# Kernel optimization log

Measured on AMD Instinct MI355X. Metric: run time of the kernel, lower is better.

Reference implementation:

```python
import jax, jax.numpy as jnp
from jax import lax
import numpy as np

B, C_IN, C_OUT, H, W, K = 4, 128, 256, 64, 64, 3
KK = K * K
MID = C_IN // 4
EPS = 1e-5


def conv2d(x, w, b, pad, groups=1):
    out = lax.conv_general_dilated(x, w, (1, 1), [(pad, pad), (pad, pad)],
                                   feature_group_count=groups,
                                   dimension_numbers=('NCHW', 'OIHW', 'NCHW'))
    return out + b[None, :, None, None]


def bnorm(x, g, b, m, v):
    # inference-mode BatchNorm2d
    scale = (g / jnp.sqrt(v + EPS))
    return (x - m[None, :, None, None]) * scale[None, :, None, None] + b[None, :, None, None]


def bilinear_gather(x, py, px):
    # x: (B,C,H,W); py/px: (B,KK,H,W) float sample coords; zero outside bounds
    Bb, C, Hh, Ww = x.shape
    xf = x.reshape(Bb, C, Hh * Ww)
    y0 = jnp.floor(py)
    x0 = jnp.floor(px)
    wy1 = py - y0
    wx1 = px - x0

    def corner(yc, xc, wgt):
        valid = (yc >= 0) & (yc <= Hh - 1) & (xc >= 0) & (xc <= Ww - 1)
        yi = jnp.clip(yc, 0, Hh - 1).astype(jnp.int32)
        xi = jnp.clip(xc, 0, Ww - 1).astype(jnp.int32)
        idx = (yi * Ww + xi).reshape(Bb, -1)  # (B, KK*H*W)
        g = jax.vmap(lambda f, i: f[:, i])(xf, idx).reshape(Bb, C, *py.shape[1:])
        return g * (wgt * valid)[:, None]

    return (corner(y0, x0, (1 - wy1) * (1 - wx1))
            + corner(y0, x0 + 1, (1 - wy1) * wx1)
            + corner(y0 + 1, x0, wy1 * (1 - wx1))
            + corner(y0 + 1, x0 + 1, wy1 * wx1))


def deform_conv2d(x, offset, mask, w, b, pad=1):
    # modulated deformable conv v2, stride=1, dilation=1, groups=1, dg=1
    Bb, C, Hh, Ww = x.shape
    off = offset.reshape(Bb, KK, 2, Hh, Ww)  # (dy,dx) per kernel point
    k = jnp.arange(KK)
    ky = (k // K).astype(x.dtype)
    kx = (k % K).astype(x.dtype)
    py = (jnp.arange(Hh, dtype=x.dtype) - pad)[None, None, :, None] + ky[None, :, None, None] + off[:, :, 0]
    px = (jnp.arange(Ww, dtype=x.dtype) - pad)[None, None, None, :] + kx[None, :, None, None] + off[:, :, 1]
    val = bilinear_gather(x, py, px) * mask[:, None]  # (B,C,KK,H,W)
    return jnp.einsum('bckhw,ock->bohw', val, w.reshape(w.shape[0], C, KK)) + b[None, :, None, None]


def setup_inputs() -> dict:
    key = jax.random.key(0)
    ks = iter(jax.random.split(key, 40))

    def P(shape, scale=0.05):
        return jax.random.normal(next(ks), shape, jnp.float32) * scale

    d = {}
    d['x'] = jax.random.normal(next(ks), (B, C_IN, H, W), jnp.float32)
    # DCConv offset branch
    d['oc1_w'] = P((MID, C_IN, 3, 3)); d['oc1_b'] = P((MID,))
    d['obn_g'] = jnp.ones((MID,)); d['obn_b'] = jnp.zeros((MID,))
    d['obn_m'] = jnp.zeros((MID,)); d['obn_v'] = jnp.ones((MID,))
    d['oc2_w'] = P((2 * KK, MID, 3, 3), 0.01); d['oc2_b'] = P((2 * KK,), 0.01)
    # DCConv mask branch
    d['mc1_w'] = P((MID, C_IN, 3, 3)); d['mc1_b'] = P((MID,))
    d['mbn_g'] = jnp.ones((MID,)); d['mbn_b'] = jnp.zeros((MID,))
    d['mbn_m'] = jnp.zeros((MID,)); d['mbn_v'] = jnp.ones((MID,))
    d['mc2_w'] = P((KK, MID, 3, 3), 0.01); d['mc2_b'] = jnp.ones((KK,))
    # DCConv main weight
    d['dc_w'] = P((C_OUT, C_IN, 3, 3)); d['dc_b'] = jnp.zeros((C_OUT,))
    # contour branch: depthwise 3x3 + BN + ReLU + 1x1
    d['cb_dw_w'] = P((C_IN, 1, 3, 3)); d['cb_dw_b'] = P((C_IN,))
    d['cbn_g'] = jnp.ones((C_IN,)); d['cbn_b'] = jnp.zeros((C_IN,))
    d['cbn_m'] = jnp.zeros((C_IN,)); d['cbn_v'] = jnp.ones((C_IN,))
    d['cb_pw_w'] = P((C_OUT // 2, C_IN, 1, 1)); d['cb_pw_b'] = P((C_OUT // 2,))
    # spatial attention 7x7 -> 1 channel
    d['sa_w'] = P((1, C_OUT + C_OUT // 2, 7, 7)); d['sa_b'] = jnp.zeros((1,))
    # fusion 1x1 + BN + ReLU
    d['fu_w'] = P((C_OUT, C_OUT + C_OUT // 2, 1, 1)); d['fu_b'] = jnp.zeros((C_OUT,))
    d['fbn_g'] = jnp.ones((C_OUT,)); d['fbn_b'] = jnp.zeros((C_OUT,))
    d['fbn_m'] = jnp.zeros((C_OUT,)); d['fbn_v'] = jnp.ones((C_OUT,))
    return d


def reference(x, oc1_w, oc1_b, obn_g, obn_b, obn_m, obn_v, oc2_w, oc2_b,
              mc1_w, mc1_b, mbn_g, mbn_b, mbn_m, mbn_v, mc2_w, mc2_b,
              dc_w, dc_b, cb_dw_w, cb_dw_b, cbn_g, cbn_b, cbn_m, cbn_v,
              cb_pw_w, cb_pw_b, sa_w, sa_b, fu_w, fu_b, fbn_g, fbn_b, fbn_m, fbn_v):
    # DCConv: offsets + sigmoid masks + modulated deformable conv
    h = jax.nn.relu(bnorm(conv2d(x, oc1_w, oc1_b, 1), obn_g, obn_b, obn_m, obn_v))
    offset = conv2d(h, oc2_w, oc2_b, 1)
    hm = jax.nn.relu(bnorm(conv2d(x, mc1_w, mc1_b, 1), mbn_g, mbn_b, mbn_m, mbn_v))
    mask = jax.nn.sigmoid(conv2d(hm, mc2_w, mc2_b, 1))
    main_feat = deform_conv2d(x, offset, mask, dc_w, dc_b, pad=1)
    # contour branch
    hc = jax.nn.relu(bnorm(conv2d(x, cb_dw_w, cb_dw_b, 1, groups=C_IN), cbn_g, cbn_b, cbn_m, cbn_v))
    contour_feat = conv2d(hc, cb_pw_w, cb_pw_b, 0)
    combined = jnp.concatenate([main_feat, contour_feat], axis=1)
    attn = jax.nn.sigmoid(conv2d(combined, sa_w, sa_b, 3))
    combined = combined * attn
    return jax.nn.relu(bnorm(conv2d(combined, fu_w, fu_b, 0), fbn_g, fbn_b, fbn_m, fbn_v))
```

## Files before the change

### kernel.cpp

```cpp
#include <hip/hip_runtime.h>
#include <hip/hip_bf16.h>
#include <math.h>

#define BN   4
#define CIN  128
#define COUT 256
#define HWP  4096

typedef __hip_bfloat16 bf16;
typedef __attribute__((ext_vector_type(8))) short sh8;
typedef __attribute__((ext_vector_type(4))) float f32x4;

__device__ __forceinline__ float b2f(bf16 v) { return __bfloat162float(v); }
__device__ __forceinline__ float bflo(unsigned u) { return __uint_as_float(u << 16); }
__device__ __forceinline__ float bfhi(unsigned u) { return __uint_as_float(u & 0xffff0000u); }
__device__ __forceinline__ unsigned short f2bfbits(float f) {
    union { bf16 h; unsigned short u; } cv; cv.h = __float2bfloat16(f); return cv.u;
}
__device__ __forceinline__ float bfj(const uint4& c, int j) {
    unsigned u = (&c.x)[j >> 1];
    return (j & 1) ? bfhi(u) : bflo(u);
}

__global__ __launch_bounds__(256) void prep_all_kernel(
    const float* __restrict__ x, bf16* __restrict__ xt,
    const float* __restrict__ dc_w,
    const float* __restrict__ oc1_w, const float* __restrict__ oc1_b,
    const float* __restrict__ obn_g, const float* __restrict__ obn_b,
    const float* __restrict__ obn_m, const float* __restrict__ obn_v,
    const float* __restrict__ mc1_w, const float* __restrict__ mc1_b,
    const float* __restrict__ mbn_g, const float* __restrict__ mbn_b,
    const float* __restrict__ mbn_m, const float* __restrict__ mbn_v,
    const float* __restrict__ fu_w, const float* __restrict__ fu_b,
    const float* __restrict__ fbn_g, const float* __restrict__ fbn_b,
    const float* __restrict__ fbn_m, const float* __restrict__ fbn_v,
    const float* __restrict__ sa_w,
    const float* __restrict__ oc2_w, const float* __restrict__ mc2_w,
    const float* __restrict__ cb_pw_w,
    const float* __restrict__ cb_dw_b, const float* __restrict__ cbn_g,
    const float* __restrict__ cbn_b, const float* __restrict__ cbn_m,
    const float* __restrict__ cbn_v,
    bf16* __restrict__ wBf2, bf16* __restrict__ wCf2, float* __restrict__ ab,
    bf16* __restrict__ wFf, bf16* __restrict__ wSAf, float* __restrict__ fab,
    bf16* __restrict__ wDf, bf16* __restrict__ wPf, float* __restrict__ dwab)
{
    __shared__ bf16 t[64][136];
    if (blockIdx.x < 256) {
        const int b = blockIdx.x >> 6, chunk = blockIdx.x & 63;
        const int pos0 = chunk * 64;
        const int tid = threadIdx.x;
        const int lane = tid & 63, wv = tid >> 6;
        const float* xb = x + (size_t)b * CIN * HWP + pos0 + lane;
        #pragma unroll 4
        for (int j = 0; j < 32; j++) {
            int ci = wv * 32 + j;
            t[lane][ci] = __float2bfloat16(xb[(size_t)ci * HWP]);
        }
        __syncthreads();
        const int p = tid >> 2, cig = tid & 3;
        uint4* dst = (uint4*)(xt + ((size_t)b * HWP + pos0 + p) * 128 + cig * 32);
        const uint4* src = (const uint4*)&t[p][cig * 32];
        #pragma unroll
        for (int q = 0; q < 4; q++) dst[q] = src[q];
        return;
    }

    int o = (blockIdx.x - 256) * 256 + threadIdx.x;
    if (o < 294912) {
        int j = o & 7, o2 = o >> 3;
        int lane = o2 & 63, t_ = o2 >> 6;
        int l16 = lane & 15, quad = lane >> 4;
        int mt = t_ & 3, t2 = t_ >> 2;
        int kt = t2 % 18, t3 = t2 / 18;
        int h = t3 & 1, wv = t3 >> 1;
        int co = wv * 64 + mt * 16 + l16;
        int kkh = kt * 32 + quad * 8 + j;
        int k = kkh >> 6, ci = h * 64 + (kkh & 63);
        wBf2[o] = __float2bfloat16(dc_w[co * 1152 + ci * 9 + k]);
    } else if (o < 368640) {
        int idx = o - 294912;
        int j = idx & 7, o2 = idx >> 3;
        int lane = o2 & 63, t_ = o2 >> 6;
        int l16 = lane & 15, quad = lane >> 4;
        int kt = t_ % 18, t2 = t_ / 18;
        int h = t2 & 1, wv = t2 >> 1;
        int co = wv * 16 + l16;
        int kkh = kt * 32 + quad * 8 + j;
        int k = kkh >> 6, ci = h * 64 + (kkh & 63);
        float v = (co < 32) ? oc1_w[co * 1152 + ci * 9 + k]
                            : mc1_w[(co - 32) * 1152 + ci * 9 + k];
        wCf2[idx] = __float2bfloat16(v);
    } else if (o < 368704) {
        int c = o - 368640;
        float g, bb, m, vv, bias;
        if (c < 32) { g = obn_g[c]; bb = obn_b[c]; m = obn_m[c]; vv = obn_v[c]; bias = oc1_b[c]; }
        else { int c2 = c - 32; g = mbn_g[c2]; bb = mbn_b[c2]; m = mbn_m[c2]; vv = mbn_v[c2]; bias = mc1_b[c2]; }
        float alpha = g / sqrtf(vv + 1e-5f);
        ab[c] = alpha;
        ab[64 + c] = (bias - m) * alpha + bb;
    } else if (o < 467008) {
        int idx = o - 368704;
        int j = idx & 7, o2 = idx >> 3;
        int lane = o2 & 63, t_ = o2 >> 6;
        int l16 = lane & 15, quad = lane >> 4;
        int mt = t_ & 3, t2 = t_ >> 2;
        int kt = t2 % 12, wv = t2 / 12;
        int co = wv * 64 + mt * 16 + l16;
        int kk = kt * 32 + quad * 8 + j;
        wFf[idx] = __float2bfloat16(fu_w[co * 384 + kk]);
    } else if (o < 491584) {
        int idx = o - 467008;
        int j = idx & 7, o2 = idx >> 3;
        int lane = o2 & 63, t_ = o2 >> 6;
        int l16 = lane & 15, quad = lane >> 4;
        int kt = t_ % 12, wv = t_ / 12;
        int jr = wv * 16 + l16;
        int kk = kt * 32 + quad * 8 + j;
        wSAf[idx] = (jr < 49) ? __float2bfloat16(sa_w[kk * 49 + jr]) : __float2bfloat16(0.f);
    } else if (o < 491840) {
        int co = o - 491584;
        float alpha = fbn_g[co] / sqrtf(fbn_v[co] + 1e-5f);
        fab[co] = alpha;
        fab[256 + co] = (fu_b[co] - fbn_m[co]) * alpha + fbn_b[co];
    } else if (o < 510272) {
        int idx = o - 491840;
        int j = idx & 7, o2 = idx >> 3;
        int lane = o2 & 63, t_ = o2 >> 6;
        int l16 = lane & 15, quad = lane >> 4;
        int mt = t_ & 1, kt = t_ >> 1;
        int co = mt * 16 + l16;
        int kk = kt * 32 + quad * 8 + j;
        int k = kk >> 6, c = kk & 63;
        float v = 0.f;
        if (co < 18 && c < 32) v = oc2_w[co * 288 + c * 9 + k];
        else if (co >= 18 && co < 27 && c >= 32) v = mc2_w[(co - 18) * 288 + (c - 32) * 9 + k];
        wDf[idx] = __float2bfloat16(v);
    } else if (o < 526656) {
        int idx = o - 510272;
        int j = idx & 7, o2 = idx >> 3;
        int lane = o2 & 63, t_ = o2 >> 6;
        int l16 = lane & 15, quad = lane >> 4;
        int wv = t_ >> 3, kt = (t_ >> 1) & 3, mt = t_ & 1;
        int co = wv * 32 + mt * 16 + l16;
        int kk = kt * 32 + quad * 8 + j;
        wPf[idx] = __float2bfloat16(cb_pw_w[co * 128 + kk]);
    } else if (o < 526784) {
        int c = o - 526656;
        float alpha = cbn_g[c] / sqrtf(cbn_v[c] + 1e-5f);
        dwab[c] = alpha;
        dwab[128 + c] = (cb_dw_b[c] - cbn_m[c]) * alpha + cbn_b[c];
    }
}

__global__ __launch_bounds__(256) void conv1_mfma_kernel(
    const bf16* __restrict__ xt, const bf16* __restrict__ wCf2, const float* __restrict__ ab,
    bf16* __restrict__ ht)
{
    __shared__ __align__(16) bf16 val[32][584];

    const int bid = blockIdx.x;
    const int b = (bid & 7) >> 1;
    const int tile = ((bid >> 3) << 1) | (bid & 1);
    const int pos0 = tile * 32;
    const int y = tile >> 1, x0 = (tile & 1) * 32;
    const int tid = threadIdx.x;
    const int lane = tid & 63, wv = tid >> 6;
    const int quad = lane >> 4, l16 = lane & 15;

    f32x4 acc[2] = {f32x4{0,0,0,0}, f32x4{0,0,0,0}};
    const bf16* xtb = xt + (size_t)b * HWP * 128;

    #pragma unroll
    for (int h = 0; h < 2; h++) {
        if (h) __syncthreads();
        {
            const int cig = tid & 7, pix = tid >> 3;
            const int ci0 = h * 64 + cig * 8;
            const int xxp = x0 + pix;
            #pragma unroll
            for (int k = 0; k < 9; k++) {
                int yy = y + k / 3 - 1, xx = xxp + k % 3 - 1;
                bool valid = (yy >= 0 && yy <= 63 && xx >= 0 && xx <= 63);
                uint4 c = {0, 0, 0, 0};
                if (valid) c = *(const uint4*)(xtb + (size_t)(yy * 64 + xx) * 128 + ci0);
                *(uint4*)&val[pix][k * 64 + cig * 8] = c;
            }
        }
        __syncthreads();

        const bf16* wl0 = wCf2 + ((size_t)(wv * 2 + h) * 18) * 512 + lane * 8;
        const bf16* vb0 = &val[l16][quad * 8];
        const bf16* vb1 = &val[16 + l16][quad * 8];
        for (int kt = 0; kt < 18; kt++) {
            sh8 af = *(const sh8*)(wl0 + kt * 512);
            sh8 b0 = *(const sh8*)(vb0 + kt * 32);
            sh8 b1 = *(const sh8*)(vb1 + kt * 32);
            acc[0] = __builtin_amdgcn_mfma_f32_16x16x32_bf16(af, b0, acc[0], 0, 0, 0);
            acc[1] = __builtin_amdgcn_mfma_f32_16x16x32_bf16(af, b1, acc[1], 0, 0, 0);
        }
    }

    const int co0 = wv * 16 + quad * 4;
    #pragma unroll
    for (int ph = 0; ph < 2; ph++) {
        float o0 = fmaxf(acc[ph][0] * ab[co0 + 0] + ab[64 + co0 + 0], 0.f);
        float o1 = fmaxf(acc[ph][1] * ab[co0 + 1] + ab[64 + co0 + 1], 0.f);
        float o2 = fmaxf(acc[ph][2] * ab[co0 + 2] + ab[64 + co0 + 2], 0.f);
        float o3 = fmaxf(acc[ph][3] * ab[co0 + 3] + ab[64 + co0 + 3], 0.f);
        uint2 pk;
        pk.x = (unsigned)f2bfbits(o0) | ((unsigned)f2bfbits(o1) << 16);
        pk.y = (unsigned)f2bfbits(o2) | ((unsigned)f2bfbits(o3) << 16);
        *(uint2*)(ht + ((size_t)b * HWP + pos0 + ph * 16 + l16) * 64 + co0) = pk;
    }
}

__global__ __launch_bounds__(256) void dwpw_kernel(
    const bf16* __restrict__ xt, const float* __restrict__ dw_w, const float* __restrict__ dwab,
    const bf16* __restrict__ wPf, const float* __restrict__ pw_b,
    const bf16* __restrict__ wSAf, bf16* __restrict__ combined, float* __restrict__ part_b)
{
    __shared__ float wl[1152];
    __shared__ float abl[256];
    __shared__ __align__(16) bf16 vdw[16][136];
    const int bid = blockIdx.x;
    const int b = bid >> 8, tile = bid & 255;
    const int pos0 = tile * 16;
    const int y = tile >> 2, x0 = (tile & 3) * 16;
    const int tid = threadIdx.x;
    for (int i = tid; i < 1152; i += 256) wl[i] = dw_w[i];
    abl[tid] = dwab[tid];
    __syncthreads();

    {
        const int cig = tid & 15, pix = tid >> 4;
        const int ci0 = cig * 8;
        const int xxp = x0 + pix;
        const bf16* xtb = xt + (size_t)b * HWP * 128;
        float g[8] = {0, 0, 0, 0, 0, 0, 0, 0};
        #pragma unroll
        for (int k = 0; k < 9; k++) {
            int yy = y + k / 3 - 1, xx = xxp + k % 3 - 1;
            if (yy < 0 || yy > 63 || xx < 0 || xx > 63) continue;
            uint4 c = *(const uint4*)(xtb + (size_t)(yy * 64 + xx) * 128 + ci0);
            #pragma unroll
            for (int j = 0; j < 8; j++)
                g[j] += wl[(ci0 + j) * 9 + k] * bfj(c, j);
        }
        uint4 pk;
        float o[8];
        #pragma unroll
        for (int j = 0; j < 8; j++)
            o[j] = fmaxf(g[j] * abl[ci0 + j] + abl[128 + ci0 + j], 0.f);
        pk.x = (unsigned)f2bfbits(o[0]) | ((unsigned)f2bfbits(o[1]) << 16);
        pk.y = (unsigned)f2bfbits(o[2]) | ((unsigned)f2bfbits(o[3]) << 16);
        pk.z = (unsigned)f2bfbits(o[4]) | ((unsigned)f2bfbits(o[5]) << 16);
        pk.w = (unsigned)f2bfbits(o[6]) | ((unsigned)f2bfbits(o[7]) << 16);
        *(uint4*)&vdw[pix][ci0] = pk;
    }
    __syncthreads();

    const int lane = tid & 63, wv = tid >> 6;
    const int quad = lane >> 4, l16 = lane & 15;
    f32x4 acc[2] = {f32x4{0,0,0,0}, f32x4{0,0,0,0}};
    const bf16* fb = &vdw[l16][quad * 8];
    const bf16* wl0 = wPf + (size_t)wv * 4096 + lane * 8;
    #pragma unroll
    for (int kt = 0; kt < 4; kt++) {
        sh8 bf = *(const sh8*)(fb + kt * 32);
        #pragma unroll
        for (int mt = 0; mt < 2; mt++) {
            sh8 af = *(const sh8*)(wl0 + (kt * 2 + mt) * 512);
            acc[mt] = __builtin_amdgcn_mfma_f32_16x16x32_bf16(af, bf, acc[mt], 0, 0, 0);
        }
    }

    bf16* ct = combined + ((size_t)b * HWP + pos0 + l16) * 384 + 256;
    #pragma unroll
    for (int mt = 0; mt < 2; mt++) {
        int co_b = wv * 32 + mt * 16 + quad * 4;
        uint2 pk;
        pk.x = (unsigned)f2bfbits(acc[mt][0] + pw_b[co_b])     | ((unsigned)f2bfbits(acc[mt][1] + pw_b[co_b + 1]) << 16);
        pk.y = (unsigned)f2bfbits(acc[mt][2] + pw_b[co_b + 2]) | ((unsigned)f2bfbits(acc[mt][3] + pw_b[co_b + 3]) << 16);
        *(uint2*)(ct + co_b) = pk;
    }

    __syncthreads();
    bf16* ct2 = &vdw[0][0];
    #pragma unroll
    for (int mt = 0; mt < 2; mt++) {
        int co_b = wv * 32 + mt * 16 + quad * 4;
        uint2 pk;
        pk.x = (unsigned)f2bfbits(acc[mt][0] + pw_b[co_b])     | ((unsigned)f2bfbits(acc[mt][1] + pw_b[co_b + 1]) << 16);
        pk.y = (unsigned)f2bfbits(acc[mt][2] + pw_b[co_b + 2]) | ((unsigned)f2bfbits(acc[mt][3] + pw_b[co_b + 3]) << 16);
        *(uint2*)(ct2 + l16 * 136 + co_b) = pk;
    }
    __syncthreads();

    f32x4 sacc = {0, 0, 0, 0};
    const bf16* awl = wSAf + (size_t)wv * 6144 + lane * 8;
    #pragma unroll
    for (int kt2 = 0; kt2 < 4; kt2++) {
        sh8 af = *(const sh8*)(awl + (8 + kt2) * 512);
        sh8 bf2 = *(const sh8*)(ct2 + l16 * 136 + kt2 * 32 + quad * 8);
        sacc = __builtin_amdgcn_mfma_f32_16x16x32_bf16(af, bf2, sacc, 0, 0, 0);
    }
    #pragma unroll
    for (int r = 0; r < 4; r++) {
        int j = wv * 16 + quad * 4 + r;
        if (j < 49) part_b[(size_t)(j * BN + b) * HWP + pos0 + l16] = sacc[r];
    }
}

__global__ __launch_bounds__(256) void deform_kernel(
    const bf16* __restrict__ xt, const bf16* __restrict__ ht, const bf16* __restrict__ wDf,
    const float* __restrict__ oc2_b, const float* __restrict__ mc2_b,
    const bf16* __restrict__ wBf2, const float* __restrict__ bias,
    const bf16* __restrict__ wSAf, bf16* __restrict__ combined, float* __restrict__ part_a)
{
    __shared__ __align__(16) bf16 val[32][584];
    __shared__ int   ti[288][4];
    __shared__ float tw[288][4];
    __shared__ float loff[18][32];
    __shared__ float lmsk[9][32];

    const int bid = blockIdx.x;
    const int b = (bid & 7) >> 1;
    const int tile = ((bid >> 3) << 1) | (bid & 1);
    const int pos0 = tile * 32;
    const int y = tile >> 1, x0 = (tile & 1) * 32;
    const int tid = threadIdx.x;
    const int lane = tid & 63, wv = tid >> 6;
    const int quad = lane >> 4, l16 = lane & 15;

    {
        const int cig = tid & 7, pix = tid >> 3;
        const int xxp = x0 + pix;
        const bf16* hb = ht + (size_t)b * HWP * 64;
        #pragma unroll
        for (int k = 0; k < 9; k++) {
            int yy = y + k / 3 - 1, xx = xxp + k % 3 - 1;
            bool valid = (yy >= 0 && yy <= 63 && xx >= 0 && xx <= 63);
            uint4 c = {0, 0, 0, 0};
            if (valid) c = *(const uint4*)(hb + (size_t)(yy * 64 + xx) * 64 + cig * 8);
            *(uint4*)&val[pix][k * 64 + cig * 8] = c;
        }
    }
    __syncthreads();
    {
        const int ph = wv >> 1, mt = wv & 1;
        f32x4 acc2 = {0, 0, 0, 0};
        const bf16* wl0 = wDf + ((size_t)mt * 64 + lane) * 8;
        const bf16* vbase = &val[ph * 16 + l16][quad * 8];
        for (int kt = 0; kt < 18; kt++) {
            sh8 af = *(const sh8*)(wl0 + kt * 1024);
            sh8 bf = *(const sh8*)(vbase + kt * 32);
            acc2 = __builtin_amdgcn_mfma_f32_16x16x32_bf16(af, bf, acc2, 0, 0, 0);
        }
        const int pix2 = ph * 16 + l16;
        #pragma unroll
        for (int r = 0; r < 4; r++) {
            int co = mt * 16 + quad * 4 + r;
            if (co < 18) {
                loff[co][pix2] = acc2[r] + oc2_b[co];
            } else if (co < 27) {
                float s = acc2[r] + mc2_b[co - 18];
                lmsk[co - 18][pix2] = 1.f / (1.f + expf(-s));
            }
        }
    }
    __syncthreads();

    for (int e = tid; e < 288; e += 256) {
        int k = e >> 5, pix = e & 31;
        int pos = pos0 + pix;
        int yp = pos >> 6, xc = pos & 63;
        float offy = loff[2 * k][pix];
        float offx = loff[2 * k + 1][pix];
        float m = lmsk[k][pix];
        float py = (float)(yp - 1 + k / 3) + offy;
        float px = (float)(xc - 1 + k % 3) + offx;
        float fy = floorf(py), fx = floorf(px);
        float wy1 = py - fy, wx1 = px - fx;
        int y0 = (int)fy, x0c = (int)fx;
        int y1 = y0 + 1, x1 = x0c + 1;
        bool vy0 = (y0 >= 0 && y0 <= 63), vy1 = (y1 >= 0 && y1 <= 63);
        bool vx0 = (x0c >= 0 && x0c <= 63), vx1 = (x1 >= 0 && x1 <= 63);
        int cy0 = min(max(y0, 0), 63), cy1 = min(max(y1, 0), 63);
        int cx0 = min(max(x0c, 0), 63), cx1 = min(max(x1, 0), 63);
        ti[e][0] = cy0 * 64 + cx0;  tw[e][0] = (vy0 && vx0) ? (1.f - wy1) * (1.f - wx1) * m : 0.f;
        ti[e][1] = cy0 * 64 + cx1;  tw[e][1] = (vy0 && vx1) ? (1.f - wy1) * wx1 * m : 0.f;
        ti[e][2] = cy1 * 64 + cx0;  tw[e][2] = (vy1 && vx0) ? wy1 * (1.f - wx1) * m : 0.f;
        ti[e][3] = cy1 * 64 + cx1;  tw[e][3] = (vy1 && vx1) ? wy1 * wx1 * m : 0.f;
    }
    __syncthreads();

    f32x4 acc[4][2] = {{f32x4{0,0,0,0}, f32x4{0,0,0,0}}, {f32x4{0,0,0,0}, f32x4{0,0,0,0}},
                       {f32x4{0,0,0,0}, f32x4{0,0,0,0}}, {f32x4{0,0,0,0}, f32x4{0,0,0,0}}};
    const bf16* xtb = xt + (size_t)b * HWP * 128;

    #pragma unroll
    for (int h = 0; h < 2; h++) {
        if (h) __syncthreads();
        {
            const int cig = tid & 7, pix = tid >> 3;
            const int ci0 = h * 64 + cig * 8;
            for (int k = 0; k < 9; k++) {
                const int e = k * 32 + pix;
                const int i0 = ti[e][0], i1 = ti[e][1], i2 = ti[e][2], i3 = ti[e][3];
                const float w0 = tw[e][0], w1 = tw[e][1], w2 = tw[e][2], w3 = tw[e][3];
                uint4 c0 = *(const uint4*)(xtb + (size_t)i0 * 128 + ci0);
                uint4 c1 = *(const uint4*)(xtb + (size_t)i1 * 128 + ci0);
                uint4 c2 = *(const uint4*)(xtb + (size_t)i2 * 128 + ci0);
                uint4 c3 = *(const uint4*)(xtb + (size_t)i3 * 128 + ci0);
                float g[8];
                #pragma unroll
                for (int j = 0; j < 8; j++)
                    g[j] = w0 * bfj(c0, j) + w1 * bfj(c1, j) + w2 * bfj(c2, j) + w3 * bfj(c3, j);
                uint4 pk;
                pk.x = (unsigned)f2bfbits(g[0]) | ((unsigned)f2bfbits(g[1]) << 16);
                pk.y = (unsigned)f2bfbits(g[2]) | ((unsigned)f2bfbits(g[3]) << 16);
                pk.z = (unsigned)f2bfbits(g[4]) | ((unsigned)f2bfbits(g[5]) << 16);
                pk.w = (unsigned)f2bfbits(g[6]) | ((unsigned)f2bfbits(g[7]) << 16);
                *(uint4*)&val[pix][k * 64 + cig * 8] = pk;
            }
        }
        __syncthreads();

        const bf16* wl0 = wBf2 + ((size_t)(wv * 2 + h) * 72) * 512 + lane * 8;
        const bf16* vb0 = &val[l16][quad * 8];
        const bf16* vb1 = &val[16 + l16][quad * 8];
        sh8 af[4], afn[4];
        #pragma unroll
        for (int mt = 0; mt < 4; mt++) af[mt] = *(const sh8*)(wl0 + mt * 512);
        for (int kt = 0; kt < 18; kt++) {
            sh8 b0 = *(const sh8*)(vb0 + kt * 32);
            sh8 b1 = *(const sh8*)(vb1 + kt * 32);
            if (kt < 17) {
                #pragma unroll
                for (int mt = 0; mt < 4; mt++)
                    afn[mt] = *(const sh8*)(wl0 + ((kt + 1) * 4 + mt) * 512);
            }
            #pragma unroll
            for (int mt = 0; mt < 4; mt++) {
                acc[mt][0] = __builtin_amdgcn_mfma_f32_16x16x32_bf16(af[mt], b0, acc[mt][0], 0, 0, 0);
                acc[mt][1] = __builtin_amdgcn_mfma_f32_16x16x32_bf16(af[mt], b1, acc[mt][1], 0, 0, 0);
            }
            #pragma unroll
            for (int mt = 0; mt < 4; mt++) af[mt] = afn[mt];
        }
    }

    uint2 pko[4][2];
    #pragma unroll
    for (int ph = 0; ph < 2; ph++) {
        bf16* ct = combined + ((size_t)b * HWP + pos0 + ph * 16 + l16) * 384;
        #pragma unroll
        for (int mt = 0; mt < 4; mt++) {
            int co_b = wv * 64 + mt * 16 + quad * 4;
            uint2 pk;
            pk.x = (unsigned)f2bfbits(acc[mt][ph][0] + bias[co_b])     | ((unsigned)f2bfbits(acc[mt][ph][1] + bias[co_b + 1]) << 16);
            pk.y = (unsigned)f2bfbits(acc[mt][ph][2] + bias[co_b + 2]) | ((unsigned)f2bfbits(acc[mt][ph][3] + bias[co_b + 3]) << 16);
            *(uint2*)(ct + co_b) = pk;
            pko[mt][ph] = pk;
        }
    }

    __syncthreads();
    bf16* ctile = &val[0][0];
    #pragma unroll
    for (int ph = 0; ph < 2; ph++) {
        int pix = ph * 16 + l16;
        #pragma unroll
        for (int mt = 0; mt < 4; mt++) {
            int co_b = wv * 64 + mt * 16 + quad * 4;
            *(uint2*)(ctile + pix * 264 + co_b) = pko[mt][ph];
        }
    }
    __syncthreads();

    f32x4 sacc[2] = {f32x4{0,0,0,0}, f32x4{0,0,0,0}};
    const bf16* awl = wSAf + (size_t)wv * 6144 + lane * 8;
    for (int kt = 0; kt < 8; kt++) {
        sh8 af = *(const sh8*)(awl + kt * 512);
        sh8 b0 = *(const sh8*)(ctile + l16 * 264 + kt * 32 + quad * 8);
        sh8 b1 = *(const sh8*)(ctile + (16 + l16) * 264 + kt * 32 + quad * 8);
        sacc[0] = __builtin_amdgcn_mfma_f32_16x16x32_bf16(af, b0, sacc[0], 0, 0, 0);
        sacc[1] = __builtin_amdgcn_mfma_f32_16x16x32_bf16(af, b1, sacc[1], 0, 0, 0);
    }
    #pragma unroll
    for (int ph = 0; ph < 2; ph++) {
        #pragma unroll
        for (int r = 0; r < 4; r++) {
            int j = wv * 16 + quad * 4 + r;
            if (j < 49) part_a[(size_t)(j * BN + b) * HWP + pos0 + ph * 16 + l16] = sacc[ph][r];
        }
    }
}

__global__ __launch_bounds__(256) void fuse_kernel(
    const bf16* __restrict__ combined, const float* __restrict__ part_a, const float* __restrict__ part_b,
    const float* __restrict__ sa_b,
    const bf16* __restrict__ wFf, const float* __restrict__ fab, float* __restrict__ out)
{
    __shared__ float sattn[16][17];
    __shared__ float lattn[16];

    const int bid = blockIdx.x;
    const int b = bid >> 8, tile = bid & 255;
    const int pos0 = tile * 16;
    const int y = tile >> 2, x0 = (tile & 3) * 16;
    const int tid = threadIdx.x;

    {
        const int px = tid & 15, g = tid >> 4;
        const int xp = x0 + px;
        float s = 0.f;
        for (int j = g; j < 49; j += 16) {
            int yy = y + j / 7 - 3, xx = xp + j % 7 - 3;
            if (yy < 0 || yy > 63 || xx < 0 || xx > 63) continue;
            size_t idx = (size_t)(j * BN + b) * HWP + yy * 64 + xx;
            s += part_a[idx] + part_b[idx];
        }
        sattn[px][g] = s;
    }
    __syncthreads();
    if (tid < 16) {
        float t = sa_b[0];
        #pragma unroll
        for (int g = 0; g < 16; g++) t += sattn[tid][g];
        lattn[tid] = 1.f / (1.f + expf(-t));
    }
    __syncthreads();

    const int lane = tid & 63, wv = tid >> 6;
    const int quad = lane >> 4, l16 = lane & 15;

    f32x4 acc[4] = {f32x4{0,0,0,0}, f32x4{0,0,0,0}, f32x4{0,0,0,0}, f32x4{0,0,0,0}};
    const bf16* fb = combined + ((size_t)b * HWP + pos0 + l16) * 384 + quad * 8;
    const bf16* wl0 = wFf + (size_t)wv * 24576 + lane * 8;

    sh8 af[4], afn[4], bf, bfn;
    bf = *(const sh8*)(fb);
    #pragma unroll
    for (int mt = 0; mt < 4; mt++) af[mt] = *(const sh8*)(wl0 + mt * 512);
    for (int kt = 0; kt < 12; kt++) {
        if (kt < 11) {
            bfn = *(const sh8*)(fb + (kt + 1) * 32);
            #pragma unroll
            for (int mt = 0; mt < 4; mt++)
                afn[mt] = *(const sh8*)(wl0 + ((kt + 1) * 4 + mt) * 512);
        }
        #pragma unroll
        for (int mt = 0; mt < 4; mt++)
            acc[mt] = __builtin_amdgcn_mfma_f32_16x16x32_bf16(af[mt], bf, acc[mt], 0, 0, 0);
        bf = bfn;
        #pragma unroll
        for (int mt = 0; mt < 4; mt++) af[mt] = afn[mt];
    }

    float a = lattn[l16];
    float* op = out + (size_t)b * COUT * HWP + pos0 + l16;
    #pragma unroll
    for (int mt = 0; mt < 4; mt++) {
        int co_b = wv * 64 + mt * 16 + quad * 4;
        #pragma unroll
        for (int r = 0; r < 4; r++) {
            int co = co_b + r;
            float o = fmaxf(acc[mt][r] * a * fab[co] + fab[256 + co], 0.f);
            op[(size_t)co * HWP] = o;
        }
    }
}

extern "C" void kernel_launch(void* const* d_in, const int* in_sizes, int n_in,
                              void* d_out, int out_size, void* d_ws, size_t ws_size,
                              hipStream_t stream)
{
    const float* x      = (const float*)d_in[0];
    const float* oc1_w  = (const float*)d_in[1];
    const float* oc1_b  = (const float*)d_in[2];
    const float* obn_g  = (const float*)d_in[3];
    const float* obn_b  = (const float*)d_in[4];
    const float* obn_m  = (const float*)d_in[5];
    const float* obn_v  = (const float*)d_in[6];
    const float* oc2_w  = (const float*)d_in[7];
    const float* oc2_b  = (const float*)d_in[8];
    const float* mc1_w  = (const float*)d_in[9];
    const float* mc1_b  = (const float*)d_in[10];
    const float* mbn_g  = (const float*)d_in[11];
    const float* mbn_b  = (const float*)d_in[12];
    const float* mbn_m  = (const float*)d_in[13];
    const float* mbn_v  = (const float*)d_in[14];
    const float* mc2_w  = (const float*)d_in[15];
    const float* mc2_b  = (const float*)d_in[16];
    const float* dc_w   = (const float*)d_in[17];
    const float* dc_b   = (const float*)d_in[18];
    const float* cb_dw_w= (const float*)d_in[19];
    const float* cb_dw_b= (const float*)d_in[20];
    const float* cbn_g  = (const float*)d_in[21];
    const float* cbn_b  = (const float*)d_in[22];
    const float* cbn_m  = (const float*)d_in[23];
    const float* cbn_v  = (const float*)d_in[24];
    const float* cb_pw_w= (const float*)d_in[25];
    const float* cb_pw_b= (const float*)d_in[26];
    const float* sa_w   = (const float*)d_in[27];
    const float* sa_b   = (const float*)d_in[28];
    const float* fu_w   = (const float*)d_in[29];
    const float* fu_b   = (const float*)d_in[30];
    const float* fbn_g  = (const float*)d_in[31];
    const float* fbn_b  = (const float*)d_in[32];
    const float* fbn_m  = (const float*)d_in[33];
    const float* fbn_v  = (const float*)d_in[34];

    bf16*  ht     = (bf16*)d_ws;
    bf16*  comb   = ht + 1048576;
    float* part_a = (float*)(comb + 6291456);
    float* part_b = part_a + 802816;
    bf16*  xt     = (bf16*)(part_b + 802816);
    bf16*  wBf2   = xt + 2097152;
    bf16*  wCf2   = wBf2 + 294912;
    float* ab     = (float*)(wCf2 + 73728);
    bf16*  wFf    = (bf16*)(ab + 128);
    bf16*  wSAf   = wFf + 98304;
    float* fab    = (float*)(wSAf + 24576);
    bf16*  wDf    = (bf16*)(fab + 512);
    bf16*  wPf    = wDf + 18432;
    float* dwab   = (float*)(wPf + 16384);

    float* out = (float*)d_out;

    prep_all_kernel<<<256 + 2058, 256, 0, stream>>>(
        x, xt,
        dc_w, oc1_w, oc1_b, obn_g, obn_b, obn_m, obn_v,
        mc1_w, mc1_b, mbn_g, mbn_b, mbn_m, mbn_v,
        fu_w, fu_b, fbn_g, fbn_b, fbn_m, fbn_v, sa_w,
        oc2_w, mc2_w, cb_pw_w, cb_dw_b, cbn_g, cbn_b, cbn_m, cbn_v,
        wBf2, wCf2, ab, wFf, wSAf, fab, wDf, wPf, dwab);
    conv1_mfma_kernel<<<512, 256, 0, stream>>>(xt, wCf2, ab, ht);
    dwpw_kernel<<<1024, 256, 0, stream>>>(xt, cb_dw_w, dwab, wPf, cb_pw_b, wSAf, comb, part_b);
    deform_kernel<<<512, 256, 0, stream>>>(xt, ht, wDf, oc2_b, mc2_b, wBf2, dc_b, wSAf, comb, part_a);
    fuse_kernel<<<1024, 256, 0, stream>>>(comb, part_a, part_b, sa_b, wFf, fab, out);
}
```

Before: 200.1 us.

## Split deform kernel output channels across two blocks per tile

The deform kernel grid doubles from 512 to 1024 blocks, and each block now computes half of the 256 output channels (128) for its 32-pixel tile. The spatial-attention partial sums are written to two separate part_a buffers, which fuse_kernel adds together. The intent is more parallelism and fewer accumulator registers per thread, which should raise occupancy. The cost is that each block pair repeats the offset/mask computation and the bilinear gather, and the workspace layout shifts. A small tweak in dwpw also reuses the packed values instead of recomputing them.

```diff
diff --git a/kernel.cpp b/kernel.cpp
--- a/kernel.cpp
+++ b/kernel.cpp
@@ -275,6 +275,7 @@
     }
 
     bf16* ct = combined + ((size_t)b * HWP + pos0 + l16) * 384 + 256;
+    uint2 pko[2];
     #pragma unroll
     for (int mt = 0; mt < 2; mt++) {
         int co_b = wv * 32 + mt * 16 + quad * 4;
@@ -282,6 +283,7 @@
         pk.x = (unsigned)f2bfbits(acc[mt][0] + pw_b[co_b])     | ((unsigned)f2bfbits(acc[mt][1] + pw_b[co_b + 1]) << 16);
         pk.y = (unsigned)f2bfbits(acc[mt][2] + pw_b[co_b + 2]) | ((unsigned)f2bfbits(acc[mt][3] + pw_b[co_b + 3]) << 16);
         *(uint2*)(ct + co_b) = pk;
+        pko[mt] = pk;
     }
 
     __syncthreads();
@@ -289,10 +291,7 @@
     #pragma unroll
     for (int mt = 0; mt < 2; mt++) {
         int co_b = wv * 32 + mt * 16 + quad * 4;
-        uint2 pk;
-        pk.x = (unsigned)f2bfbits(acc[mt][0] + pw_b[co_b])     | ((unsigned)f2bfbits(acc[mt][1] + pw_b[co_b + 1]) << 16);
-        pk.y = (unsigned)f2bfbits(acc[mt][2] + pw_b[co_b + 2]) | ((unsigned)f2bfbits(acc[mt][3] + pw_b[co_b + 3]) << 16);
-        *(uint2*)(ct2 + l16 * 136 + co_b) = pk;
+        *(uint2*)(ct2 + l16 * 136 + co_b) = pko[mt];
     }
     __syncthreads();
 
@@ -325,7 +324,9 @@
 
     const int bid = blockIdx.x;
     const int b = (bid & 7) >> 1;
-    const int tile = ((bid >> 3) << 1) | (bid & 1);
+    const int rest = bid >> 3;
+    const int ch = rest & 1;
+    const int tile = (((rest >> 1) << 1) | (bid & 1));
     const int pos0 = tile * 32;
     const int y = tile >> 1, x0 = (tile & 1) * 32;
     const int tid = threadIdx.x;
@@ -394,9 +395,10 @@
     }
     __syncthreads();
 
-    f32x4 acc[4][2] = {{f32x4{0,0,0,0}, f32x4{0,0,0,0}}, {f32x4{0,0,0,0}, f32x4{0,0,0,0}},
-                       {f32x4{0,0,0,0}, f32x4{0,0,0,0}}, {f32x4{0,0,0,0}, f32x4{0,0,0,0}}};
+    f32x4 acc[2][2] = {{f32x4{0,0,0,0}, f32x4{0,0,0,0}}, {f32x4{0,0,0,0}, f32x4{0,0,0,0}}};
     const bf16* xtb = xt + (size_t)b * HWP * 128;
+    const int wv_o = ch * 2 + (wv >> 1);
+    const int mtb = (wv & 1) * 2;
 
     #pragma unroll
     for (int h = 0; h < 2; h++) {
@@ -426,42 +428,42 @@
         }
         __syncthreads();
 
-        const bf16* wl0 = wBf2 + ((size_t)(wv * 2 + h) * 72) * 512 + lane * 8;
+        const bf16* wl0 = wBf2 + ((size_t)(wv_o * 2 + h) * 72) * 512 + lane * 8;
         const bf16* vb0 = &val[l16][quad * 8];
         const bf16* vb1 = &val[16 + l16][quad * 8];
-        sh8 af[4], afn[4];
-        #pragma unroll
-        for (int mt = 0; mt < 4; mt++) af[mt] = *(const sh8*)(wl0 + mt * 512);
+        sh8 af[2], afn[2];
+        #pragma unroll
+        for (int m2 = 0; m2 < 2; m2++) af[m2] = *(const sh8*)(wl0 + (mtb + m2) * 512);
         for (int kt = 0; kt < 18; kt++) {
             sh8 b0 = *(const sh8*)(vb0 + kt * 32);
             sh8 b1 = *(const sh8*)(vb1 + kt * 32);
             if (kt < 17) {
                 #pragma unroll
-                for (int mt = 0; mt < 4; mt++)
-                    afn[mt] = *(const sh8*)(wl0 + ((kt + 1) * 4 + mt) * 512);
+                for (int m2 = 0; m2 < 2; m2++)
+                    afn[m2] = *(const sh8*)(wl0 + ((kt + 1) * 4 + mtb + m2) * 512);
             }
             #pragma unroll
-            for (int mt = 0; mt < 4; mt++) {
-                acc[mt][0] = __builtin_amdgcn_mfma_f32_16x16x32_bf16(af[mt], b0, acc[mt][0], 0, 0, 0);
-                acc[mt][1] = __builtin_amdgcn_mfma_f32_16x16x32_bf16(af[mt], b1, acc[mt][1], 0, 0, 0);
+            for (int m2 = 0; m2 < 2; m2++) {
+                acc[m2][0] = __builtin_amdgcn_mfma_f32_16x16x32_bf16(af[m2], b0, acc[m2][0], 0, 0, 0);
+                acc[m2][1] = __builtin_amdgcn_mfma_f32_16x16x32_bf16(af[m2], b1, acc[m2][1], 0, 0, 0);
             }
             #pragma unroll
-            for (int mt = 0; mt < 4; mt++) af[mt] = afn[mt];
-        }
-    }
-
-    uint2 pko[4][2];
+            for (int m2 = 0; m2 < 2; m2++) af[m2] = afn[m2];
+        }
+    }
+
+    uint2 pko[2][2];
     #pragma unroll
     for (int ph = 0; ph < 2; ph++) {
         bf16* ct = combined + ((size_t)b * HWP + pos0 + ph * 16 + l16) * 384;
         #pragma unroll
-        for (int mt = 0; mt < 4; mt++) {
-            int co_b = wv * 64 + mt * 16 + quad * 4;
+        for (int m2 = 0; m2 < 2; m2++) {
+            int co = ch * 128 + wv * 32 + m2 * 16 + quad * 4;
             uint2 pk;
-            pk.x = (unsigned)f2bfbits(acc[mt][ph][0] + bias[co_b])     | ((unsigned)f2bfbits(acc[mt][ph][1] + bias[co_b + 1]) << 16);
-            pk.y = (unsigned)f2bfbits(acc[mt][ph][2] + bias[co_b + 2]) | ((unsigned)f2bfbits(acc[mt][ph][3] + bias[co_b + 3]) << 16);
-            *(uint2*)(ct + co_b) = pk;
-            pko[mt][ph] = pk;
+            pk.x = (unsigned)f2bfbits(acc[m2][ph][0] + bias[co])     | ((unsigned)f2bfbits(acc[m2][ph][1] + bias[co + 1]) << 16);
+            pk.y = (unsigned)f2bfbits(acc[m2][ph][2] + bias[co + 2]) | ((unsigned)f2bfbits(acc[m2][ph][3] + bias[co + 3]) << 16);
+            *(uint2*)(ct + co) = pk;
+            pko[m2][ph] = pk;
         }
     }
 
@@ -471,28 +473,30 @@
     for (int ph = 0; ph < 2; ph++) {
         int pix = ph * 16 + l16;
         #pragma unroll
-        for (int mt = 0; mt < 4; mt++) {
-            int co_b = wv * 64 + mt * 16 + quad * 4;
-            *(uint2*)(ctile + pix * 264 + co_b) = pko[mt][ph];
+        for (int m2 = 0; m2 < 2; m2++) {
+            int col = wv * 32 + m2 * 16 + quad * 4;
+            *(uint2*)(ctile + pix * 136 + col) = pko[m2][ph];
         }
     }
     __syncthreads();
 
     f32x4 sacc[2] = {f32x4{0,0,0,0}, f32x4{0,0,0,0}};
     const bf16* awl = wSAf + (size_t)wv * 6144 + lane * 8;
-    for (int kt = 0; kt < 8; kt++) {
-        sh8 af = *(const sh8*)(awl + kt * 512);
-        sh8 b0 = *(const sh8*)(ctile + l16 * 264 + kt * 32 + quad * 8);
-        sh8 b1 = *(const sh8*)(ctile + (16 + l16) * 264 + kt * 32 + quad * 8);
+    #pragma unroll
+    for (int kt2 = 0; kt2 < 4; kt2++) {
+        sh8 af = *(const sh8*)(awl + (ch * 4 + kt2) * 512);
+        sh8 b0 = *(const sh8*)(ctile + l16 * 136 + kt2 * 32 + quad * 8);
+        sh8 b1 = *(const sh8*)(ctile + (16 + l16) * 136 + kt2 * 32 + quad * 8);
         sacc[0] = __builtin_amdgcn_mfma_f32_16x16x32_bf16(af, b0, sacc[0], 0, 0, 0);
         sacc[1] = __builtin_amdgcn_mfma_f32_16x16x32_bf16(af, b1, sacc[1], 0, 0, 0);
     }
+    float* pa = part_a + (size_t)ch * 802816;
     #pragma unroll
     for (int ph = 0; ph < 2; ph++) {
         #pragma unroll
         for (int r = 0; r < 4; r++) {
             int j = wv * 16 + quad * 4 + r;
-            if (j < 49) part_a[(size_t)(j * BN + b) * HWP + pos0 + ph * 16 + l16] = sacc[ph][r];
+            if (j < 49) pa[(size_t)(j * BN + b) * HWP + pos0 + ph * 16 + l16] = sacc[ph][r];
         }
     }
 }
@@ -519,7 +523,7 @@
             int yy = y + j / 7 - 3, xx = xp + j % 7 - 3;
             if (yy < 0 || yy > 63 || xx < 0 || xx > 63) continue;
             size_t idx = (size_t)(j * BN + b) * HWP + yy * 64 + xx;
-            s += part_a[idx] + part_b[idx];
+            s += part_a[idx] + part_a[idx + 802816] + part_b[idx];
         }
         sattn[px][g] = s;
     }
@@ -615,7 +619,7 @@
     bf16*  ht     = (bf16*)d_ws;
     bf16*  comb   = ht + 1048576;
     float* part_a = (float*)(comb + 6291456);
-    float* part_b = part_a + 802816;
+    float* part_b = part_a + 1605632;
     bf16*  xt     = (bf16*)(part_b + 802816);
     bf16*  wBf2   = xt + 2097152;
     bf16*  wCf2   = wBf2 + 294912;
@@ -638,6 +642,6 @@
         wBf2, wCf2, ab, wFf, wSAf, fab, wDf, wPf, dwab);
     conv1_mfma_kernel<<<512, 256, 0, stream>>>(xt, wCf2, ab, ht);
     dwpw_kernel<<<1024, 256, 0, stream>>>(xt, cb_dw_w, dwab, wPf, cb_pw_b, wSAf, comb, part_b);
-    deform_kernel<<<512, 256, 0, stream>>>(xt, ht, wDf, oc2_b, mc2_b, wBf2, dc_b, wSAf, comb, part_a);
+    deform_kernel<<<1024, 256, 0, stream>>>(xt, ht, wDf, oc2_b, mc2_b, wBf2, dc_b, wSAf, comb, part_a);
     fuse_kernel<<<1024, 256, 0, stream>>>(comb, part_a, part_b, sa_b, wFf, fab, out);
 }
```

After: 207.1 us. 3.5% more time.
